# Optimization experiments

Hardware: AMD Instinct MI355X
Metric: run time of the kernel (lower is better)

The kernel has to match this reference:

```python
import jax, jax.numpy as jnp
import numpy as np

HIDDEN = 1024
NUM_HEAD = 16
HEAD_DIM = HIDDEN // NUM_HEAD


def setup_inputs() -> dict:
    key = jax.random.key(0)
    ks = jax.random.split(key, 12)
    bs, seq = 4, 2048
    inp = {
        'srcQ': jax.random.normal(ks[0], (bs, seq, HIDDEN), jnp.float32),
        'srcK': jax.random.normal(ks[1], (bs, seq, HIDDEN), jnp.float32),
        'srcV': jax.random.normal(ks[2], (bs, seq, HIDDEN), jnp.float32),
        'mask': jnp.ones((bs, 1, 1, seq), jnp.int32),
        'Wq': jax.random.normal(ks[3], (HIDDEN, HIDDEN), jnp.float32) * 0.02,
        'bq': jnp.zeros((HIDDEN,), jnp.float32),
        'Wk': jax.random.normal(ks[4], (HIDDEN, HIDDEN), jnp.float32) * 0.02,
        'bk': jnp.zeros((HIDDEN,), jnp.float32),
        'Wv': jax.random.normal(ks[5], (HIDDEN, HIDDEN), jnp.float32) * 0.02,
        'bv': jnp.zeros((HIDDEN,), jnp.float32),
        'Wo': jax.random.normal(ks[6], (HIDDEN, HIDDEN), jnp.float32) * 0.02,
        'bo': jnp.zeros((HIDDEN,), jnp.float32),
    }
    return inp


def _split_heads(x):
    # [bs, seq, hidden] -> [bs, num_head, seq, head_dim]
    bs, seq, _ = x.shape
    return x.reshape(bs, seq, NUM_HEAD, HEAD_DIM).transpose(0, 2, 1, 3)


def reference(srcQ, srcK, srcV, mask, Wq, bq, Wk, bk, Wv, bv, Wo, bo):
    Q = _split_heads(srcQ @ Wq + bq)
    K = _split_heads(srcK @ Wk + bk)
    V = _split_heads(srcV @ Wv + bv)
    # NOTE: original module applies NO 1/sqrt(d) scaling (scale tensor unused)
    scores = jnp.einsum('bhqd,bhkd->bhqk', Q, K)
    scores = jnp.where(mask == 0, jnp.float32(-10000.0), scores)
    attn = jax.nn.softmax(scores, axis=-1)  # dropout is identity in eval
    out = jnp.einsum('bhqk,bhkd->bhqd', attn, V)
    bs, _, seq, _ = out.shape
    out = out.transpose(0, 2, 1, 3).reshape(bs, seq, HIDDEN)
    return out @ Wo + bo
```

## Files before the change

kernel.cpp:

```cpp
#include <hip/hip_runtime.h>

typedef short bf16x8 __attribute__((ext_vector_type(8)));
typedef short bf16x4 __attribute__((ext_vector_type(4)));
typedef float f32x4 __attribute__((ext_vector_type(4)));
typedef unsigned short ushort8 __attribute__((ext_vector_type(8)));
typedef unsigned short ushort4v __attribute__((ext_vector_type(4)));
typedef unsigned int uint4v __attribute__((ext_vector_type(4)));
typedef float float4v __attribute__((ext_vector_type(4)));

#define LOG2E 1.4426950408889634f
#define MASKED_VAL -14426.950408889634f

__device__ __forceinline__ unsigned short f2bf(float f) {
  unsigned u = __builtin_bit_cast(unsigned, f);
  u = u + 0x7fffu + ((u >> 16) & 1u);
  return (unsigned short)(u >> 16);
}

__device__ __forceinline__ unsigned pk2(float a, float b) {
  unsigned r;
  asm("v_cvt_pk_bf16_f32 %0, %1, %2" : "=v"(r) : "v"(a), "v"(b));
  return r;
}

__device__ __forceinline__ float exp2a(float x) {
  float r;
  asm("v_exp_f32 %0, %1" : "=v"(r) : "v"(x));
  return r;
}

__device__ __forceinline__ void gload16(const void* g, void* l) {
  __builtin_amdgcn_global_load_lds(
      (const __attribute__((address_space(1))) unsigned int*)g,
      (__attribute__((address_space(3))) unsigned int*)l, 16, 0, 0);
}

__device__ __forceinline__ void store_out(float* p, float v) { *p = v; }
__device__ __forceinline__ void store_out(unsigned short* p, float v) { *p = f2bf(v); }

__global__ __launch_bounds__(256) void transpose_w4(const float* __restrict__ W0,
                                                    const float* __restrict__ W1,
                                                    const float* __restrict__ W2,
                                                    const float* __restrict__ W3,
                                                    unsigned short* __restrict__ Wt) {
  __shared__ float tile[32][33];
  const int z = blockIdx.z;
  const float* W = (z == 0) ? W0 : (z == 1) ? W1 : (z == 2) ? W2 : W3;
  unsigned short* o = Wt + (size_t)z * (1 << 20);
  int bx = blockIdx.x * 32;
  int by = blockIdx.y * 32;
  int tx = threadIdx.x & 31;
  int ty = threadIdx.x >> 5;
#pragma unroll
  for (int j = 0; j < 32; j += 8)
    tile[ty + j][tx] = W[(size_t)(by + ty + j) * 1024 + bx + tx];
  __syncthreads();
#pragma unroll
  for (int j = 0; j < 32; j += 8)
    o[(size_t)(bx + ty + j) * 1024 + by + tx] = f2bf(tile[tx][ty + j]);
}

__global__ __launch_bounds__(256, 4) void gemm_qkv(
    const float* __restrict__ srcQ, const float* __restrict__ srcK,
    const float* __restrict__ srcV, const unsigned short* __restrict__ Wt,
    const float* __restrict__ bq, const float* __restrict__ bk,
    const float* __restrict__ bv, unsigned short* __restrict__ Qb,
    unsigned short* __restrict__ Kb, unsigned short* __restrict__ Vt) {
  __shared__ __align__(16) unsigned short As[2][128 * 32];
  __shared__ __align__(16) unsigned short Bs[2][128 * 32];
  const int K = 1024, N = 1024;
  const int chunk = blockIdx.x >> 9;
  const int inner = blockIdx.x & 511;
  const int x = inner & 7, i = inner >> 3;
  const int bm = (x << 3) + (i >> 3);
  const int bn = i & 7;
  const float* Af = (chunk == 0) ? srcQ : (chunk == 1) ? srcK : srcV;
  const unsigned short* Bt = Wt + (size_t)chunk * (1 << 20);
  const float* bias = (chunk == 0) ? bq : (chunk == 1) ? bk : bv;
  const float scale = (chunk == 0) ? LOG2E : 1.0f;
  const int t = threadIdx.x;
  const int lane = t & 63, wid = t >> 6;
  const int wr = wid >> 1, wc = wid & 1;
  const int lr = lane & 15, lg = lane >> 4;
  f32x4 acc[4][4] = {};
  const size_t baseA = (size_t)(bm * 128) * K;
  const size_t baseB = (size_t)(bn * 128) * K;
  const int c0 = t, c1 = t + 256;
  const int rA0 = c0 >> 2, kA0 = (c0 & 3) * 8;
  const int rA1 = c1 >> 2, kA1 = (c1 & 3) * 8;
  const size_t a0off = baseA + (size_t)rA0 * K + kA0;
  const size_t a1off = baseA + (size_t)rA1 * K + kA1;
  const size_t b0off = baseB + (size_t)rA0 * K + kA0;
  const size_t b1off = baseB + (size_t)rA1 * K + kA1;

  {
    float4v f0 = *(const float4v*)&Af[a0off];
    float4v f1 = *(const float4v*)&Af[a0off + 4];
    float4v f2 = *(const float4v*)&Af[a1off];
    float4v f3 = *(const float4v*)&Af[a1off + 4];
    gload16(&Bt[b0off], &Bs[0][c0 * 8]);
    gload16(&Bt[b1off], &Bs[0][c1 * 8]);
    uint4v w0, w1;
    w0[0] = pk2(f0[0], f0[1]); w0[1] = pk2(f0[2], f0[3]);
    w0[2] = pk2(f1[0], f1[1]); w0[3] = pk2(f1[2], f1[3]);
    w1[0] = pk2(f2[0], f2[1]); w1[1] = pk2(f2[2], f2[3]);
    w1[2] = pk2(f3[0], f3[1]); w1[3] = pk2(f3[2], f3[3]);
    *(uint4v*)&As[0][c0 * 8] = w0;
    *(uint4v*)&As[0][c1 * 8] = w1;
  }
  __syncthreads();

  int cur = 0;
  for (int ks = 0; ks < K; ks += 32) {
    const int nxt = cur ^ 1;
    const bool more = (ks + 32) < K;
    float4v f0, f1, f2, f3;
    if (more) {
      f0 = *(const float4v*)&Af[a0off + ks + 32];
      f1 = *(const float4v*)&Af[a0off + ks + 36];
      f2 = *(const float4v*)&Af[a1off + ks + 32];
      f3 = *(const float4v*)&Af[a1off + ks + 36];
      gload16(&Bt[b0off + ks + 32], &Bs[nxt][c0 * 8]);
      gload16(&Bt[b1off + ks + 32], &Bs[nxt][c1 * 8]);
    }
    bf16x8 a[4], b[4];
#pragma unroll
    for (int m = 0; m < 4; ++m)
      a[m] = *(const bf16x8*)&As[cur][(wr * 64 + 16 * m + lr) * 32 + lg * 8];
#pragma unroll
    for (int n = 0; n < 4; ++n)
      b[n] = *(const bf16x8*)&Bs[cur][(wc * 64 + 16 * n + lr) * 32 + lg * 8];
#pragma unroll
    for (int m = 0; m < 4; ++m)
#pragma unroll
      for (int n = 0; n < 4; ++n)
        acc[m][n] = __builtin_amdgcn_mfma_f32_16x16x32_bf16(a[m], b[n], acc[m][n], 0, 0, 0);
    if (more) {
      uint4v w0, w1;
      w0[0] = pk2(f0[0], f0[1]); w0[1] = pk2(f0[2], f0[3]);
      w0[2] = pk2(f1[0], f1[1]); w0[3] = pk2(f1[2], f1[3]);
      w1[0] = pk2(f2[0], f2[1]); w1[1] = pk2(f2[2], f2[3]);
      w1[2] = pk2(f3[0], f3[1]); w1[3] = pk2(f3[2], f3[3]);
      *(uint4v*)&As[nxt][c0 * 8] = w0;
      *(uint4v*)&As[nxt][c1 * 8] = w1;
    }
    __syncthreads();
    cur = nxt;
  }
  const int rowb = bm * 128 + wr * 64;
  const int colb = bn * 128 + wc * 64;
  if (chunk == 2) {
    const int bidx = rowb >> 11;
    const int srow = rowb & 2047;
#pragma unroll
    for (int n = 0; n < 4; ++n) {
      int col = colb + 16 * n + lr;
      float bv_ = bias[col];
#pragma unroll
      for (int m = 0; m < 4; ++m) {
        int s0 = srow + 16 * m + 4 * lg;
        ushort4v u;
#pragma unroll
        for (int r = 0; r < 4; ++r) u[r] = f2bf(acc[m][n][r] + bv_);
        *(ushort4v*)&Vt[((size_t)(bidx * 1024 + col)) * 2048 + s0] = u;
      }
    }
  } else {
    unsigned short* C = (chunk == 0) ? Qb : Kb;
#pragma unroll
    for (int n = 0; n < 4; ++n) {
      int col = colb + 16 * n + lr;
      float bv_ = bias[col];
#pragma unroll
      for (int m = 0; m < 4; ++m) {
        int row0 = rowb + 16 * m + 4 * lg;
#pragma unroll
        for (int r = 0; r < 4; ++r)
          C[(size_t)(row0 + r) * N + col] = f2bf((acc[m][n][r] + bv_) * scale);
      }
    }
  }
}

template <typename OT>
__global__ __launch_bounds__(256, 4) void gemm_bt(const unsigned short* __restrict__ A,
                                                  const unsigned short* __restrict__ Bt,
                                                  const float* __restrict__ bias,
                                                  OT* __restrict__ C, int M, int N, int K) {
  __shared__ __align__(16) unsigned short As[2][128 * 32];
  __shared__ __align__(16) unsigned short Bs[2][128 * 32];
  const int t = threadIdx.x;
  const int nb = N >> 7;
  int bm, bn;
  if ((M >> 7) == 64 && nb == 8) {
    int x = blockIdx.x & 7, i = blockIdx.x >> 3;
    bm = (x << 3) + (i >> 3);
    bn = i & 7;
  } else {
    bm = blockIdx.x / nb;
    bn = blockIdx.x % nb;
  }
  const int lane = t & 63, wid = t >> 6;
  const int wr = wid >> 1, wc = wid & 1;
  const int lr = lane & 15, lg = lane >> 4;
  f32x4 acc[4][4] = {};
  const size_t baseA = (size_t)(bm * 128) * K;
  const size_t baseB = (size_t)(bn * 128) * K;
  const int c0 = t, c1 = t + 256;
  const int rA0 = c0 >> 2, kA0 = (c0 & 3) * 8;
  const int rA1 = c1 >> 2, kA1 = (c1 & 3) * 8;
  const size_t a0off = baseA + (size_t)rA0 * K + kA0;
  const size_t a1off = baseA + (size_t)rA1 * K + kA1;
  const size_t b0off = baseB + (size_t)rA0 * K + kA0;
  const size_t b1off = baseB + (size_t)rA1 * K + kA1;

  gload16(&A[a0off], &As[0][c0 * 8]);
  gload16(&A[a1off], &As[0][c1 * 8]);
  gload16(&Bt[b0off], &Bs[0][c0 * 8]);
  gload16(&Bt[b1off], &Bs[0][c1 * 8]);
  __syncthreads();

  int cur = 0;
  for (int ks = 0; ks < K; ks += 32) {
    const int nxt = cur ^ 1;
    if (ks + 32 < K) {
      gload16(&A[a0off + ks + 32], &As[nxt][c0 * 8]);
      gload16(&A[a1off + ks + 32], &As[nxt][c1 * 8]);
      gload16(&Bt[b0off + ks + 32], &Bs[nxt][c0 * 8]);
      gload16(&Bt[b1off + ks + 32], &Bs[nxt][c1 * 8]);
    }
    bf16x8 a[4], b[4];
#pragma unroll
    for (int m = 0; m < 4; ++m)
      a[m] = *(const bf16x8*)&As[cur][(wr * 64 + 16 * m + lr) * 32 + lg * 8];
#pragma unroll
    for (int n = 0; n < 4; ++n)
      b[n] = *(const bf16x8*)&Bs[cur][(wc * 64 + 16 * n + lr) * 32 + lg * 8];
#pragma unroll
    for (int m = 0; m < 4; ++m)
#pragma unroll
      for (int n = 0; n < 4; ++n)
        acc[m][n] = __builtin_amdgcn_mfma_f32_16x16x32_bf16(a[m], b[n], acc[m][n], 0, 0, 0);
    __syncthreads();
    cur = nxt;
  }
  const int rowb = bm * 128 + wr * 64;
  const int colb = bn * 128 + wc * 64;
#pragma unroll
  for (int n = 0; n < 4; ++n) {
    int col = colb + 16 * n + lr;
    float bv = bias[col];
#pragma unroll
    for (int m = 0; m < 4; ++m) {
      int row0 = rowb + 16 * m + 4 * lg;
#pragma unroll
      for (int r = 0; r < 4; ++r) {
        float v = acc[m][n][r] + bv;
        store_out(&C[(size_t)(row0 + r) * N + col], v);
      }
    }
  }
}

__global__ __launch_bounds__(256, 4) void attn_kernel(
    const unsigned short* __restrict__ Q, const unsigned short* __restrict__ K,
    const unsigned short* __restrict__ V, const int* __restrict__ mask,
    unsigned short* __restrict__ ctx) {
  __shared__ __align__(16) unsigned short pool[16384];
  __shared__ int s_any[4];
  unsigned short* Kbuf0 = pool;
  unsigned short* Kbuf1 = pool + 4096;
  unsigned short* Vbuf0 = pool + 8192;
  unsigned short* Vbuf1 = pool + 12288;
  const int g = blockIdx.x;
  const int bid = (g & 7) * 128 + (g >> 3);
  const int qb = bid & 15, h = (bid >> 4) & 15, b = bid >> 8;
  const int t = threadIdx.x;
  const int lane = t & 63, wid = t >> 6;
  const int lr = lane & 15, lg = lane >> 4;
  const size_t rowQ0 = (size_t)(b * 2048 + qb * 128);
  const int hcol = h * 64;
  const size_t vrow0 = (size_t)((b * 16 + h) * 64) * 2048;

  size_t ksrc[2], vsrc[2];
  int ldso[2];
#pragma unroll
  for (int i = 0; i < 2; ++i) {
    int ci = t + 256 * i;
    int row = ci >> 3, pos = ci & 7;
    ksrc[i] = (size_t)(b * 2048 + row) * 1024 + hcol + ((pos ^ (row & 7)) << 3);
    vsrc[i] = vrow0 + (size_t)row * 2048 + ((pos ^ ((row >> 1) & 7)) << 3);
    ldso[i] = ci * 8;
  }
#pragma unroll
  for (int i = 0; i < 4; ++i) {
    int ci = t + 256 * i;
    int row = ci >> 3, pos = ci & 7;
    gload16(&Q[(rowQ0 + row) * 1024 + hcol + ((pos ^ (row & 7)) << 3)], &pool[ci * 8]);
  }
  int bad = 0;
  const int* mb = mask + b * 2048;
#pragma unroll
  for (int i = 0; i < 2; ++i) {
    int4 mv = *(const int4*)&mb[t * 8 + i * 4];
    bad |= (mv.x == 0) | (mv.y == 0) | (mv.z == 0) | (mv.w == 0);
  }
  unsigned long long bb = __ballot(bad);
  if (lane == 0) s_any[wid] = (bb != 0ULL);
  __syncthreads();
  bf16x8 aq[2][2];
#pragma unroll
  for (int m = 0; m < 2; ++m)
#pragma unroll
    for (int kd = 0; kd < 2; ++kd) {
      int row = wid * 32 + 16 * m + lr;
      int ch = (4 * kd + lg) ^ (lr & 7);
      aq[m][kd] = *(const bf16x8*)&pool[row * 64 + ch * 8];
    }
  const bool anymask = (s_any[0] | s_any[1] | s_any[2] | s_any[3]) != 0;
  __syncthreads();
#pragma unroll
  for (int i = 0; i < 2; ++i) gload16(&K[ksrc[i]], &Kbuf0[ldso[i]]);
#pragma unroll
  for (int i = 0; i < 2; ++i) gload16(&V[vsrc[i]], &Vbuf0[ldso[i]]);
  __syncthreads();

  f32x4 o[2][4] = {};
  f32x4 ol[2] = {};
  const short oneb = 0x3F80;
  const bf16x8 ones8 = {oneb, oneb, oneb, oneb, oneb, oneb, oneb, oneb};
  const f32x4 zero4 = {0.f, 0.f, 0.f, 0.f};
  const int ch0 = (lg ^ (lr & 7)) * 8;
  const int ch1 = ((4 + lg) ^ (lr & 7)) * 8;
  const int sw = lr >> 1;

  for (int kb = 0; kb < 32; ++kb) {
    const int bi = kb & 1;
    const unsigned short* Kb_ = bi ? Kbuf1 : Kbuf0;
    const unsigned short* Vb_ = bi ? Vbuf1 : Vbuf0;
    unsigned short* Kn_ = bi ? Kbuf0 : Kbuf1;
    unsigned short* Vn_ = bi ? Vbuf0 : Vbuf1;
    if (kb + 1 < 32) {
      const size_t ko = (size_t)(kb + 1) * 64 * 1024;
      const size_t vo = (size_t)(kb + 1) * 64;
#pragma unroll
      for (int i = 0; i < 2; ++i) gload16(&K[ksrc[i] + ko], &Kn_[ldso[i]]);
#pragma unroll
      for (int i = 0; i < 2; ++i) gload16(&V[vsrc[i] + vo], &Vn_[ldso[i]]);
    }
    f32x4 s[2][4];
    __builtin_amdgcn_s_setprio(1);
#pragma unroll
    for (int n = 0; n < 4; ++n) {
      bf16x8 k0 = *(const bf16x8*)&Kb_[(16 * n + lr) * 64 + ch0];
      bf16x8 k1 = *(const bf16x8*)&Kb_[(16 * n + lr) * 64 + ch1];
      f32x4 t0 = __builtin_amdgcn_mfma_f32_16x16x32_bf16(k0, aq[0][0], zero4, 0, 0, 0);
      s[0][n] = __builtin_amdgcn_mfma_f32_16x16x32_bf16(k1, aq[0][1], t0, 0, 0, 0);
      f32x4 t1 = __builtin_amdgcn_mfma_f32_16x16x32_bf16(k0, aq[1][0], zero4, 0, 0, 0);
      s[1][n] = __builtin_amdgcn_mfma_f32_16x16x32_bf16(k1, aq[1][1], t1, 0, 0, 0);
    }
    __builtin_amdgcn_s_setprio(0);
    if (anymask) {
      const int* mrow = mb + kb * 64;
#pragma unroll
      for (int n = 0; n < 4; ++n) {
        int4 mv = *(const int4*)&mrow[16 * n + 4 * lg];
        int mm[4] = {mv.x, mv.y, mv.z, mv.w};
#pragma unroll
        for (int r = 0; r < 4; ++r)
          if (mm[r] == 0) { s[0][n][r] = MASKED_VAL; s[1][n][r] = MASKED_VAL; }
      }
    }
#pragma unroll
    for (int m = 0; m < 2; ++m)
#pragma unroll
      for (int n = 0; n < 4; ++n)
#pragma unroll
        for (int r = 0; r < 4; ++r) s[m][n][r] = exp2a(s[m][n][r]);
#pragma unroll
    for (int kk = 0; kk < 2; ++kk) {
      bf16x8 pf[2];
#pragma unroll
      for (int m = 0; m < 2; ++m) {
        uint4v u;
        u[0] = pk2(s[m][2 * kk][0], s[m][2 * kk][1]);
        u[1] = pk2(s[m][2 * kk][2], s[m][2 * kk][3]);
        u[2] = pk2(s[m][2 * kk + 1][0], s[m][2 * kk + 1][1]);
        u[3] = pk2(s[m][2 * kk + 1][2], s[m][2 * kk + 1][3]);
        pf[m] = __builtin_bit_cast(bf16x8, u);
      }
      __builtin_amdgcn_s_setprio(1);
      ol[0] = __builtin_amdgcn_mfma_f32_16x16x32_bf16(ones8, pf[0], ol[0], 0, 0, 0);
      ol[1] = __builtin_amdgcn_mfma_f32_16x16x32_bf16(ones8, pf[1], ol[1], 0, 0, 0);
      const int p0 = (4 * kk + (lg >> 1)) ^ sw;
      const int base0 = lr * 64 + p0 * 8 + (lg & 1) * 4;
      const int base1 = lr * 64 + (p0 ^ 2) * 8 + (lg & 1) * 4;
#pragma unroll
      for (int dn = 0; dn < 4; ++dn) {
        bf16x4 v0 = *(const bf16x4*)&Vb_[base0 + dn * 1024];
        bf16x4 v1 = *(const bf16x4*)&Vb_[base1 + dn * 1024];
        bf16x8 vb = __builtin_shufflevector(v0, v1, 0, 1, 2, 3, 4, 5, 6, 7);
#pragma unroll
        for (int m = 0; m < 2; ++m)
          o[m][dn] = __builtin_amdgcn_mfma_f32_16x16x32_bf16(vb, pf[m], o[m][dn], 0, 0, 0);
      }
      __builtin_amdgcn_s_setprio(0);
    }
    __syncthreads();
  }
#pragma unroll
  for (int m = 0; m < 2; ++m) {
    float inv = 1.f / ol[m][0];
    size_t q = rowQ0 + wid * 32 + 16 * m + lr;
#pragma unroll
    for (int dn = 0; dn < 4; ++dn) {
      ushort4v u;
#pragma unroll
      for (int r = 0; r < 4; ++r) u[r] = f2bf(o[m][dn][r] * inv);
      *(ushort4v*)&ctx[q * 1024 + hcol + 16 * dn + 4 * lg] = u;
    }
  }
}

extern "C" void kernel_launch(void* const* d_in, const int* in_sizes, int n_in,
                              void* d_out, int out_size, void* d_ws, size_t ws_size,
                              hipStream_t stream) {
  const float* srcQ = (const float*)d_in[0];
  const float* srcK = (const float*)d_in[1];
  const float* srcV = (const float*)d_in[2];
  const int*   mask = (const int*)d_in[3];
  const float* Wq = (const float*)d_in[4];
  const float* bq = (const float*)d_in[5];
  const float* Wk = (const float*)d_in[6];
  const float* bk = (const float*)d_in[7];
  const float* Wv = (const float*)d_in[8];
  const float* bv = (const float*)d_in[9];
  const float* Wo = (const float*)d_in[10];
  const float* bo = (const float*)d_in[11];
  float* out = (float*)d_out;

  const int M = 8192, N = 1024, Kd = 1024;
  char* ws = (char*)d_ws;
  unsigned short* ctx = (unsigned short*)(ws);
  unsigned short* Qb  = (unsigned short*)(ws + (size_t)(16 << 20));
  unsigned short* Kb  = (unsigned short*)(ws + (size_t)(32 << 20));
  unsigned short* Vt  = (unsigned short*)(ws + (size_t)(48 << 20));
  unsigned short* Wt  = (unsigned short*)(ws + (size_t)(64 << 20));

  transpose_w4<<<dim3(32, 32, 4), 256, 0, stream>>>(Wq, Wk, Wv, Wo, Wt);

  gemm_qkv<<<1536, 256, 0, stream>>>(srcQ, srcK, srcV, Wt, bq, bk, bv, Qb, Kb, Vt);

  attn_kernel<<<1024, 256, 0, stream>>>(Qb, Kb, Vt, mask, ctx);

  gemm_bt<float><<<(M / 128) * (N / 128), 256, 0, stream>>>(ctx, Wt + 3 * (1 << 20), bo, out, M, N, Kd);
}
```

Baseline: 188.8 us.

## Software-pipeline attention loop: overlap QK of next tile with PV of previous

Restructures the attention main loop so each iteration does QK for block kb and PV for block kb-1, with softmax output carried across iterations and V triple-buffered. Even and odd waves issue QK and PV in opposite order so the exp/softmax work of one wave can overlap MFMA work of another. The mask check becomes a per-wave __any, which removes a shared array and a barrier, and offsets move to 32-bit. This costs more LDS (an extra V buffer) and keeps more P fragments live in registers, which could lower occupancy.

```diff
diff --git a/kernel.cpp b/kernel.cpp
--- a/kernel.cpp
+++ b/kernel.cpp
@@ -266,12 +266,8 @@
     const unsigned short* __restrict__ Q, const unsigned short* __restrict__ K,
     const unsigned short* __restrict__ V, const int* __restrict__ mask,
     unsigned short* __restrict__ ctx) {
-  __shared__ __align__(16) unsigned short pool[16384];
-  __shared__ int s_any[4];
-  unsigned short* Kbuf0 = pool;
-  unsigned short* Kbuf1 = pool + 4096;
-  unsigned short* Vbuf0 = pool + 8192;
-  unsigned short* Vbuf1 = pool + 12288;
+  __shared__ __align__(16) unsigned short Kpool[2][4096];
+  __shared__ __align__(16) unsigned short Vpool[3][4096];
   const int g = blockIdx.x;
   const int bid = (g & 7) * 128 + (g >> 3);
   const int qb = bid & 15, h = (bid >> 4) & 15, b = bid >> 8;
@@ -280,33 +276,37 @@
   const int lr = lane & 15, lg = lane >> 4;
   const size_t rowQ0 = (size_t)(b * 2048 + qb * 128);
   const int hcol = h * 64;
-  const size_t vrow0 = (size_t)((b * 16 + h) * 64) * 2048;
-
-  size_t ksrc[2], vsrc[2];
+  const unsigned vrow0 = (unsigned)((b * 16 + h) * 64) * 2048u;
+
+  unsigned ksrc[2], vsrc[2];
   int ldso[2];
 #pragma unroll
   for (int i = 0; i < 2; ++i) {
     int ci = t + 256 * i;
     int row = ci >> 3, pos = ci & 7;
-    ksrc[i] = (size_t)(b * 2048 + row) * 1024 + hcol + ((pos ^ (row & 7)) << 3);
-    vsrc[i] = vrow0 + (size_t)row * 2048 + ((pos ^ ((row >> 1) & 7)) << 3);
+    ksrc[i] = (unsigned)((b * 2048 + row) * 1024 + hcol + ((pos ^ (row & 7)) << 3));
+    vsrc[i] = vrow0 + (unsigned)row * 2048u + (unsigned)((pos ^ ((row >> 1) & 7)) << 3);
     ldso[i] = ci * 8;
   }
+  unsigned short* Kflat = &Kpool[0][0];
 #pragma unroll
   for (int i = 0; i < 4; ++i) {
     int ci = t + 256 * i;
     int row = ci >> 3, pos = ci & 7;
-    gload16(&Q[(rowQ0 + row) * 1024 + hcol + ((pos ^ (row & 7)) << 3)], &pool[ci * 8]);
-  }
+    gload16(&Q[(rowQ0 + row) * 1024 + hcol + ((pos ^ (row & 7)) << 3)], &Kflat[ci * 8]);
+  }
+#pragma unroll
+  for (int i = 0; i < 2; ++i) gload16(&V[vsrc[i]], &Vpool[0][ldso[i]]);
+#pragma unroll
+  for (int i = 0; i < 2; ++i) gload16(&V[vsrc[i] + 64], &Vpool[1][ldso[i]]);
   int bad = 0;
   const int* mb = mask + b * 2048;
 #pragma unroll
-  for (int i = 0; i < 2; ++i) {
-    int4 mv = *(const int4*)&mb[t * 8 + i * 4];
+  for (int i = 0; i < 8; ++i) {
+    int4 mv = *(const int4*)&mb[lane * 32 + i * 4];
     bad |= (mv.x == 0) | (mv.y == 0) | (mv.z == 0) | (mv.w == 0);
   }
-  unsigned long long bb = __ballot(bad);
-  if (lane == 0) s_any[wid] = (bb != 0ULL);
+  const bool anymask = __any(bad);
   __syncthreads();
   bf16x8 aq[2][2];
 #pragma unroll
@@ -315,14 +315,11 @@
     for (int kd = 0; kd < 2; ++kd) {
       int row = wid * 32 + 16 * m + lr;
       int ch = (4 * kd + lg) ^ (lr & 7);
-      aq[m][kd] = *(const bf16x8*)&pool[row * 64 + ch * 8];
-    }
-  const bool anymask = (s_any[0] | s_any[1] | s_any[2] | s_any[3]) != 0;
-  __syncthreads();
-#pragma unroll
-  for (int i = 0; i < 2; ++i) gload16(&K[ksrc[i]], &Kbuf0[ldso[i]]);
-#pragma unroll
-  for (int i = 0; i < 2; ++i) gload16(&V[vsrc[i]], &Vbuf0[ldso[i]]);
+      aq[m][kd] = *(const bf16x8*)&Kflat[row * 64 + ch * 8];
+    }
+  __syncthreads();
+#pragma unroll
+  for (int i = 0; i < 2; ++i) gload16(&K[ksrc[i]], &Kpool[0][ldso[i]]);
   __syncthreads();
 
   f32x4 o[2][4] = {};
@@ -334,21 +331,16 @@
   const int ch1 = ((4 + lg) ^ (lr & 7)) * 8;
   const int sw = lr >> 1;
 
-  for (int kb = 0; kb < 32; ++kb) {
-    const int bi = kb & 1;
-    const unsigned short* Kb_ = bi ? Kbuf1 : Kbuf0;
-    const unsigned short* Vb_ = bi ? Vbuf1 : Vbuf0;
-    unsigned short* Kn_ = bi ? Kbuf0 : Kbuf1;
-    unsigned short* Vn_ = bi ? Vbuf0 : Vbuf1;
-    if (kb + 1 < 32) {
-      const size_t ko = (size_t)(kb + 1) * 64 * 1024;
-      const size_t vo = (size_t)(kb + 1) * 64;
-#pragma unroll
-      for (int i = 0; i < 2; ++i) gload16(&K[ksrc[i] + ko], &Kn_[ldso[i]]);
-#pragma unroll
-      for (int i = 0; i < 2; ++i) gload16(&V[vsrc[i] + vo], &Vn_[ldso[i]]);
-    }
-    f32x4 s[2][4];
+  unsigned short* kC = &Kpool[0][0];
+  unsigned short* kN = &Kpool[1][0];
+  unsigned short* vA = &Vpool[0][0];
+  unsigned short* vB = &Vpool[1][0];
+  unsigned short* vC = &Vpool[2][0];
+
+  f32x4 s[2][4];
+  bf16x8 pf[2][2];
+
+  auto QK = [&](const unsigned short* Kb_) {
     __builtin_amdgcn_s_setprio(1);
 #pragma unroll
     for (int n = 0; n < 4; ++n) {
@@ -360,6 +352,27 @@
       s[1][n] = __builtin_amdgcn_mfma_f32_16x16x32_bf16(k1, aq[1][1], t1, 0, 0, 0);
     }
     __builtin_amdgcn_s_setprio(0);
+  };
+  auto PV = [&](const unsigned short* Vb_) {
+    __builtin_amdgcn_s_setprio(1);
+#pragma unroll
+    for (int kk = 0; kk < 2; ++kk) {
+      const int p0 = (4 * kk + (lg >> 1)) ^ sw;
+      const int base0 = lr * 64 + p0 * 8 + (lg & 1) * 4;
+      const int base1 = lr * 64 + (p0 ^ 2) * 8 + (lg & 1) * 4;
+#pragma unroll
+      for (int dn = 0; dn < 4; ++dn) {
+        bf16x4 v0 = *(const bf16x4*)&Vb_[base0 + dn * 1024];
+        bf16x4 v1 = *(const bf16x4*)&Vb_[base1 + dn * 1024];
+        bf16x8 vb = __builtin_shufflevector(v0, v1, 0, 1, 2, 3, 4, 5, 6, 7);
+#pragma unroll
+        for (int m = 0; m < 2; ++m)
+          o[m][dn] = __builtin_amdgcn_mfma_f32_16x16x32_bf16(vb, pf[kk][m], o[m][dn], 0, 0, 0);
+      }
+    }
+    __builtin_amdgcn_s_setprio(0);
+  };
+  auto SOFTMAX = [&](int kb) {
     if (anymask) {
       const int* mrow = mb + kb * 64;
 #pragma unroll
@@ -379,7 +392,6 @@
         for (int r = 0; r < 4; ++r) s[m][n][r] = exp2a(s[m][n][r]);
 #pragma unroll
     for (int kk = 0; kk < 2; ++kk) {
-      bf16x8 pf[2];
 #pragma unroll
       for (int m = 0; m < 2; ++m) {
         uint4v u;
@@ -387,27 +399,43 @@
         u[1] = pk2(s[m][2 * kk][2], s[m][2 * kk][3]);
         u[2] = pk2(s[m][2 * kk + 1][0], s[m][2 * kk + 1][1]);
         u[3] = pk2(s[m][2 * kk + 1][2], s[m][2 * kk + 1][3]);
-        pf[m] = __builtin_bit_cast(bf16x8, u);
-      }
-      __builtin_amdgcn_s_setprio(1);
-      ol[0] = __builtin_amdgcn_mfma_f32_16x16x32_bf16(ones8, pf[0], ol[0], 0, 0, 0);
-      ol[1] = __builtin_amdgcn_mfma_f32_16x16x32_bf16(ones8, pf[1], ol[1], 0, 0, 0);
-      const int p0 = (4 * kk + (lg >> 1)) ^ sw;
-      const int base0 = lr * 64 + p0 * 8 + (lg & 1) * 4;
-      const int base1 = lr * 64 + (p0 ^ 2) * 8 + (lg & 1) * 4;
-#pragma unroll
-      for (int dn = 0; dn < 4; ++dn) {
-        bf16x4 v0 = *(const bf16x4*)&Vb_[base0 + dn * 1024];
-        bf16x4 v1 = *(const bf16x4*)&Vb_[base1 + dn * 1024];
-        bf16x8 vb = __builtin_shufflevector(v0, v1, 0, 1, 2, 3, 4, 5, 6, 7);
-#pragma unroll
-        for (int m = 0; m < 2; ++m)
-          o[m][dn] = __builtin_amdgcn_mfma_f32_16x16x32_bf16(vb, pf[m], o[m][dn], 0, 0, 0);
-      }
-      __builtin_amdgcn_s_setprio(0);
-    }
+        pf[kk][m] = __builtin_bit_cast(bf16x8, u);
+      }
+      ol[0] = __builtin_amdgcn_mfma_f32_16x16x32_bf16(ones8, pf[kk][0], ol[0], 0, 0, 0);
+      ol[1] = __builtin_amdgcn_mfma_f32_16x16x32_bf16(ones8, pf[kk][1], ol[1], 0, 0, 0);
+    }
+  };
+
+#pragma unroll
+  for (int i = 0; i < 2; ++i) gload16(&K[ksrc[i] + 65536u], &kN[ldso[i]]);
+  QK(kC);
+  SOFTMAX(0);
+  __syncthreads();
+  { unsigned short* tk = kC; kC = kN; kN = tk; }
+
+  for (int kb = 1; kb < 32; ++kb) {
+    if (kb < 31) {
+      const unsigned ko = (unsigned)(kb + 1) * 65536u;
+      const unsigned vo = (unsigned)(kb + 1) * 64u;
+#pragma unroll
+      for (int i = 0; i < 2; ++i) gload16(&K[ksrc[i] + ko], &kN[ldso[i]]);
+#pragma unroll
+      for (int i = 0; i < 2; ++i) gload16(&V[vsrc[i] + vo], &vC[ldso[i]]);
+    }
+    if ((wid & 1) == 0) {
+      QK(kC);
+      PV(vA);
+    } else {
+      PV(vA);
+      QK(kC);
+    }
+    SOFTMAX(kb);
     __syncthreads();
-  }
+    { unsigned short* tk = kC; kC = kN; kN = tk; }
+    { unsigned short* tv = vA; vA = vB; vB = vC; vC = tv; }
+  }
+  PV(vA);
+
 #pragma unroll
   for (int m = 0; m < 2; ++m) {
     float inv = 1.f / ol[m][0];
```

Result: slower. 212.6 us (+12.6%).

## Triple-buffer LDS in QKV and output GEMMs with deeper prefetch and priority hints

Applied to the files above, without the earlier changes.

Both projection GEMMs move from double to triple LDS buffers with rotating pointers. Loads are issued two k-steps ahead, and waits use explicit vmcnt/lgkmcnt with raw s_barrier instead of __syncthreads. MFMA sections are wrapped in s_setprio, and the QKV kernel keeps two register sets of fp32 A data in flight. The intent is to hide global load latency; the cost is more LDS per block (launch bounds lowered to 3 waves) and more register pressure.

```diff
diff --git a/kernel.cpp b/kernel.cpp
--- a/kernel.cpp
+++ b/kernel.cpp
@@ -34,9 +34,6 @@
       (const __attribute__((address_space(1))) unsigned int*)g,
       (__attribute__((address_space(3))) unsigned int*)l, 16, 0, 0);
 }
-
-__device__ __forceinline__ void store_out(float* p, float v) { *p = v; }
-__device__ __forceinline__ void store_out(unsigned short* p, float v) { *p = f2bf(v); }
 
 __global__ __launch_bounds__(256) void transpose_w4(const float* __restrict__ W0,
                                                     const float* __restrict__ W1,
@@ -60,14 +57,14 @@
     o[(size_t)(bx + ty + j) * 1024 + by + tx] = f2bf(tile[tx][ty + j]);
 }
 
-__global__ __launch_bounds__(256, 4) void gemm_qkv(
+__global__ __launch_bounds__(256, 3) void gemm_qkv(
     const float* __restrict__ srcQ, const float* __restrict__ srcK,
     const float* __restrict__ srcV, const unsigned short* __restrict__ Wt,
     const float* __restrict__ bq, const float* __restrict__ bk,
     const float* __restrict__ bv, unsigned short* __restrict__ Qb,
     unsigned short* __restrict__ Kb, unsigned short* __restrict__ Vt) {
-  __shared__ __align__(16) unsigned short As[2][128 * 32];
-  __shared__ __align__(16) unsigned short Bs[2][128 * 32];
+  __shared__ __align__(16) unsigned short As[3][128 * 32];
+  __shared__ __align__(16) unsigned short Bs[3][128 * 32];
   const int K = 1024, N = 1024;
   const int chunk = blockIdx.x >> 9;
   const int inner = blockIdx.x & 511;
@@ -86,67 +83,93 @@
   const size_t baseA = (size_t)(bm * 128) * K;
   const size_t baseB = (size_t)(bn * 128) * K;
   const int c0 = t, c1 = t + 256;
-  const int rA0 = c0 >> 2, kA0 = (c0 & 3) * 8;
-  const int rA1 = c1 >> 2, kA1 = (c1 & 3) * 8;
-  const size_t a0off = baseA + (size_t)rA0 * K + kA0;
-  const size_t a1off = baseA + (size_t)rA1 * K + kA1;
-  const size_t b0off = baseB + (size_t)rA0 * K + kA0;
-  const size_t b1off = baseB + (size_t)rA1 * K + kA1;
-
-  {
-    float4v f0 = *(const float4v*)&Af[a0off];
-    float4v f1 = *(const float4v*)&Af[a0off + 4];
-    float4v f2 = *(const float4v*)&Af[a1off];
-    float4v f3 = *(const float4v*)&Af[a1off + 4];
-    gload16(&Bt[b0off], &Bs[0][c0 * 8]);
-    gload16(&Bt[b1off], &Bs[0][c1 * 8]);
+  const size_t a0off = baseA + (size_t)(c0 >> 2) * K + (c0 & 3) * 8;
+  const size_t a1off = baseA + (size_t)(c1 >> 2) * K + (c1 & 3) * 8;
+  const size_t b0off = baseB + (size_t)(c0 >> 2) * K + (c0 & 3) * 8;
+  const size_t b1off = baseB + (size_t)(c1 >> 2) * K + (c1 & 3) * 8;
+
+  unsigned short* pA0 = &As[0][0];
+  unsigned short* pA1 = &As[1][0];
+  unsigned short* pA2 = &As[2][0];
+  unsigned short* pB0 = &Bs[0][0];
+  unsigned short* pB1 = &Bs[1][0];
+  unsigned short* pB2 = &Bs[2][0];
+  float4v fE[4], fO[4];
+
+  auto loadA = [&](float4v* f, int ks) {
+    f[0] = *(const float4v*)&Af[a0off + ks];
+    f[1] = *(const float4v*)&Af[a0off + ks + 4];
+    f[2] = *(const float4v*)&Af[a1off + ks];
+    f[3] = *(const float4v*)&Af[a1off + ks + 4];
+  };
+  auto writeA = [&](const float4v* f, unsigned short* dst) {
     uint4v w0, w1;
-    w0[0] = pk2(f0[0], f0[1]); w0[1] = pk2(f0[2], f0[3]);
-    w0[2] = pk2(f1[0], f1[1]); w0[3] = pk2(f1[2], f1[3]);
-    w1[0] = pk2(f2[0], f2[1]); w1[1] = pk2(f2[2], f2[3]);
-    w1[2] = pk2(f3[0], f3[1]); w1[3] = pk2(f3[2], f3[3]);
-    *(uint4v*)&As[0][c0 * 8] = w0;
-    *(uint4v*)&As[0][c1 * 8] = w1;
-  }
-  __syncthreads();
-
-  int cur = 0;
-  for (int ks = 0; ks < K; ks += 32) {
-    const int nxt = cur ^ 1;
-    const bool more = (ks + 32) < K;
-    float4v f0, f1, f2, f3;
-    if (more) {
-      f0 = *(const float4v*)&Af[a0off + ks + 32];
-      f1 = *(const float4v*)&Af[a0off + ks + 36];
-      f2 = *(const float4v*)&Af[a1off + ks + 32];
-      f3 = *(const float4v*)&Af[a1off + ks + 36];
-      gload16(&Bt[b0off + ks + 32], &Bs[nxt][c0 * 8]);
-      gload16(&Bt[b1off + ks + 32], &Bs[nxt][c1 * 8]);
-    }
+    w0[0] = pk2(f[0][0], f[0][1]); w0[1] = pk2(f[0][2], f[0][3]);
+    w0[2] = pk2(f[1][0], f[1][1]); w0[3] = pk2(f[1][2], f[1][3]);
+    w1[0] = pk2(f[2][0], f[2][1]); w1[1] = pk2(f[2][2], f[2][3]);
+    w1[2] = pk2(f[3][0], f[3][1]); w1[3] = pk2(f[3][2], f[3][3]);
+    *(uint4v*)&dst[c0 * 8] = w0;
+    *(uint4v*)&dst[c1 * 8] = w1;
+  };
+  auto compute = [&]() {
     bf16x8 a[4], b[4];
 #pragma unroll
     for (int m = 0; m < 4; ++m)
-      a[m] = *(const bf16x8*)&As[cur][(wr * 64 + 16 * m + lr) * 32 + lg * 8];
+      a[m] = *(const bf16x8*)&pA0[(wr * 64 + 16 * m + lr) * 32 + lg * 8];
 #pragma unroll
     for (int n = 0; n < 4; ++n)
-      b[n] = *(const bf16x8*)&Bs[cur][(wc * 64 + 16 * n + lr) * 32 + lg * 8];
+      b[n] = *(const bf16x8*)&pB0[(wc * 64 + 16 * n + lr) * 32 + lg * 8];
+    __builtin_amdgcn_s_setprio(1);
 #pragma unroll
     for (int m = 0; m < 4; ++m)
 #pragma unroll
       for (int n = 0; n < 4; ++n)
         acc[m][n] = __builtin_amdgcn_mfma_f32_16x16x32_bf16(a[m], b[n], acc[m][n], 0, 0, 0);
-    if (more) {
-      uint4v w0, w1;
-      w0[0] = pk2(f0[0], f0[1]); w0[1] = pk2(f0[2], f0[3]);
-      w0[2] = pk2(f1[0], f1[1]); w0[3] = pk2(f1[2], f1[3]);
-      w1[0] = pk2(f2[0], f2[1]); w1[1] = pk2(f2[2], f2[3]);
-      w1[2] = pk2(f3[0], f3[1]); w1[3] = pk2(f3[2], f3[3]);
-      *(uint4v*)&As[nxt][c0 * 8] = w0;
-      *(uint4v*)&As[nxt][c1 * 8] = w1;
-    }
-    __syncthreads();
-    cur = nxt;
-  }
+    __builtin_amdgcn_s_setprio(0);
+  };
+  auto rotate = [&]() {
+    unsigned short* ta = pA0; pA0 = pA1; pA1 = pA2; pA2 = ta;
+    unsigned short* tb = pB0; pB0 = pB1; pB1 = pB2; pB2 = tb;
+  };
+
+  gload16(&Bt[b0off], &pB0[c0 * 8]);
+  gload16(&Bt[b1off], &pB0[c1 * 8]);
+  loadA(fE, 0);
+  gload16(&Bt[b0off + 32], &pB1[c0 * 8]);
+  gload16(&Bt[b1off + 32], &pB1[c1 * 8]);
+  loadA(fO, 32);
+  writeA(fE, pA0);
+  asm volatile("s_waitcnt lgkmcnt(0)" ::: "memory");
+  __builtin_amdgcn_s_barrier();
+
+  for (int it = 0; it < 16; ++it) {
+    const int ks0 = 64 * it;
+    if (it < 15) {
+      gload16(&Bt[b0off + ks0 + 64], &pB2[c0 * 8]);
+      gload16(&Bt[b1off + ks0 + 64], &pB2[c1 * 8]);
+      loadA(fE, ks0 + 64);
+    }
+    compute();
+    writeA(fO, pA1);
+    asm volatile("s_waitcnt lgkmcnt(0)" ::: "memory");
+    __builtin_amdgcn_sched_barrier(0);
+    __builtin_amdgcn_s_barrier();
+    rotate();
+    if (it < 15) {
+      gload16(&Bt[b0off + ks0 + 96], &pB2[c0 * 8]);
+      gload16(&Bt[b1off + ks0 + 96], &pB2[c1 * 8]);
+      loadA(fO, ks0 + 96);
+    }
+    compute();
+    if (it < 15) {
+      writeA(fE, pA1);
+      asm volatile("s_waitcnt lgkmcnt(0)" ::: "memory");
+      __builtin_amdgcn_sched_barrier(0);
+      __builtin_amdgcn_s_barrier();
+      rotate();
+    }
+  }
+
   const int rowb = bm * 128 + wr * 64;
   const int colb = bn * 128 + wc * 64;
   if (chunk == 2) {
@@ -182,24 +205,17 @@
   }
 }
 
-template <typename OT>
-__global__ __launch_bounds__(256, 4) void gemm_bt(const unsigned short* __restrict__ A,
-                                                  const unsigned short* __restrict__ Bt,
-                                                  const float* __restrict__ bias,
-                                                  OT* __restrict__ C, int M, int N, int K) {
-  __shared__ __align__(16) unsigned short As[2][128 * 32];
-  __shared__ __align__(16) unsigned short Bs[2][128 * 32];
+__global__ __launch_bounds__(256, 3) void gemm_out(const unsigned short* __restrict__ A,
+                                                   const unsigned short* __restrict__ Bt,
+                                                   const float* __restrict__ bias,
+                                                   float* __restrict__ C) {
+  __shared__ __align__(16) unsigned short As[3][128 * 32];
+  __shared__ __align__(16) unsigned short Bs[3][128 * 32];
+  const int K = 1024, N = 1024;
+  const int x = blockIdx.x & 7, i = blockIdx.x >> 3;
+  const int bm = (x << 3) + (i >> 3);
+  const int bn = i & 7;
   const int t = threadIdx.x;
-  const int nb = N >> 7;
-  int bm, bn;
-  if ((M >> 7) == 64 && nb == 8) {
-    int x = blockIdx.x & 7, i = blockIdx.x >> 3;
-    bm = (x << 3) + (i >> 3);
-    bn = i & 7;
-  } else {
-    bm = blockIdx.x / nb;
-    bn = blockIdx.x % nb;
-  }
   const int lane = t & 63, wid = t >> 6;
   const int wr = wid >> 1, wc = wid & 1;
   const int lr = lane & 15, lg = lane >> 4;
@@ -207,43 +223,63 @@
   const size_t baseA = (size_t)(bm * 128) * K;
   const size_t baseB = (size_t)(bn * 128) * K;
   const int c0 = t, c1 = t + 256;
-  const int rA0 = c0 >> 2, kA0 = (c0 & 3) * 8;
-  const int rA1 = c1 >> 2, kA1 = (c1 & 3) * 8;
-  const size_t a0off = baseA + (size_t)rA0 * K + kA0;
-  const size_t a1off = baseA + (size_t)rA1 * K + kA1;
-  const size_t b0off = baseB + (size_t)rA0 * K + kA0;
-  const size_t b1off = baseB + (size_t)rA1 * K + kA1;
-
-  gload16(&A[a0off], &As[0][c0 * 8]);
-  gload16(&A[a1off], &As[0][c1 * 8]);
-  gload16(&Bt[b0off], &Bs[0][c0 * 8]);
-  gload16(&Bt[b1off], &Bs[0][c1 * 8]);
-  __syncthreads();
-
-  int cur = 0;
-  for (int ks = 0; ks < K; ks += 32) {
-    const int nxt = cur ^ 1;
-    if (ks + 32 < K) {
-      gload16(&A[a0off + ks + 32], &As[nxt][c0 * 8]);
-      gload16(&A[a1off + ks + 32], &As[nxt][c1 * 8]);
-      gload16(&Bt[b0off + ks + 32], &Bs[nxt][c0 * 8]);
-      gload16(&Bt[b1off + ks + 32], &Bs[nxt][c1 * 8]);
-    }
+  const size_t a0off = baseA + (size_t)(c0 >> 2) * K + (c0 & 3) * 8;
+  const size_t a1off = baseA + (size_t)(c1 >> 2) * K + (c1 & 3) * 8;
+  const size_t b0off = baseB + (size_t)(c0 >> 2) * K + (c0 & 3) * 8;
+  const size_t b1off = baseB + (size_t)(c1 >> 2) * K + (c1 & 3) * 8;
+
+  unsigned short* pA0 = &As[0][0];
+  unsigned short* pA1 = &As[1][0];
+  unsigned short* pA2 = &As[2][0];
+  unsigned short* pB0 = &Bs[0][0];
+  unsigned short* pB1 = &Bs[1][0];
+  unsigned short* pB2 = &Bs[2][0];
+
+  auto issue = [&](int ks, unsigned short* dA, unsigned short* dB) {
+    gload16(&A[a0off + ks], &dA[c0 * 8]);
+    gload16(&A[a1off + ks], &dA[c1 * 8]);
+    gload16(&Bt[b0off + ks], &dB[c0 * 8]);
+    gload16(&Bt[b1off + ks], &dB[c1 * 8]);
+  };
+  auto rotate = [&]() {
+    unsigned short* ta = pA0; pA0 = pA1; pA1 = pA2; pA2 = ta;
+    unsigned short* tb = pB0; pB0 = pB1; pB1 = pB2; pB2 = tb;
+  };
+
+  issue(0, pA0, pB0);
+  issue(32, pA1, pB1);
+  asm volatile("s_waitcnt vmcnt(4)" ::: "memory");
+  __builtin_amdgcn_sched_barrier(0);
+  __builtin_amdgcn_s_barrier();
+
+  for (int tt = 0; tt < 32; ++tt) {
+    if (tt < 30) issue(32 * tt + 64, pA2, pB2);
     bf16x8 a[4], b[4];
 #pragma unroll
     for (int m = 0; m < 4; ++m)
-      a[m] = *(const bf16x8*)&As[cur][(wr * 64 + 16 * m + lr) * 32 + lg * 8];
+      a[m] = *(const bf16x8*)&pA0[(wr * 64 + 16 * m + lr) * 32 + lg * 8];
 #pragma unroll
     for (int n = 0; n < 4; ++n)
-      b[n] = *(const bf16x8*)&Bs[cur][(wc * 64 + 16 * n + lr) * 32 + lg * 8];
+      b[n] = *(const bf16x8*)&pB0[(wc * 64 + 16 * n + lr) * 32 + lg * 8];
+    __builtin_amdgcn_s_setprio(1);
 #pragma unroll
     for (int m = 0; m < 4; ++m)
 #pragma unroll
       for (int n = 0; n < 4; ++n)
         acc[m][n] = __builtin_amdgcn_mfma_f32_16x16x32_bf16(a[m], b[n], acc[m][n], 0, 0, 0);
-    __syncthreads();
-    cur = nxt;
-  }
+    __builtin_amdgcn_s_setprio(0);
+    if (tt < 31) {
+      if (tt < 30) {
+        asm volatile("s_waitcnt vmcnt(4)" ::: "memory");
+      } else {
+        asm volatile("s_waitcnt vmcnt(0)" ::: "memory");
+      }
+      __builtin_amdgcn_sched_barrier(0);
+      __builtin_amdgcn_s_barrier();
+      rotate();
+    }
+  }
+
   const int rowb = bm * 128 + wr * 64;
   const int colb = bn * 128 + wc * 64;
 #pragma unroll
@@ -254,10 +290,8 @@
     for (int m = 0; m < 4; ++m) {
       int row0 = rowb + 16 * m + 4 * lg;
 #pragma unroll
-      for (int r = 0; r < 4; ++r) {
-        float v = acc[m][n][r] + bv;
-        store_out(&C[(size_t)(row0 + r) * N + col], v);
-      }
+      for (int r = 0; r < 4; ++r)
+        C[(size_t)(row0 + r) * N + col] = acc[m][n][r] + bv;
     }
   }
 }
@@ -439,7 +473,6 @@
   const float* bo = (const float*)d_in[11];
   float* out = (float*)d_out;
 
-  const int M = 8192, N = 1024, Kd = 1024;
   char* ws = (char*)d_ws;
   unsigned short* ctx = (unsigned short*)(ws);
   unsigned short* Qb  = (unsigned short*)(ws + (size_t)(16 << 20));
@@ -453,5 +486,5 @@
 
   attn_kernel<<<1024, 256, 0, stream>>>(Qb, Kb, Vt, mask, ctx);
 
-  gemm_bt<float><<<(M / 128) * (N / 128), 256, 0, stream>>>(ctx, Wt + 3 * (1 << 20), bo, out, M, N, Kd);
-}
+  gemm_out<<<512, 256, 0, stream>>>(ctx, Wt + 3 * (1 << 20), bo, out);
+}
```

Result: faster. 180.9 us (-4.2%).
